# Kernel optimization log

Hardware: AMD Instinct MI355X
Metric: run time of the kernel (lower is better)

The kernel has to match this reference:

```python
import jax, jax.numpy as jnp
import numpy as np

D_MODEL = 512
DK = 4
DV = 8
HIDD = 10
HEAD = D_MODEL // DV  # 64
LN_EPS = 1e-5


def setup_inputs() -> dict:
    key = jax.random.key(0)
    ks = jax.random.split(key, 10)
    B, S, Se = 8, 512, 512
    u = jax.random.uniform  # torch.rand initializer for attention weights
    n = jax.random.normal
    return {
        "x": n(ks[0], (B, S, D_MODEL), jnp.float32),
        "x_enc": n(ks[1], (B, Se, D_MODEL), jnp.float32),
        "WqM": u(ks[2], (D_MODEL, HEAD * DK), jnp.float32),
        "WkM": u(ks[3], (D_MODEL, HEAD * DK), jnp.float32),
        "WvM": u(ks[4], (D_MODEL, HEAD * DV), jnp.float32),
        "ln_g": jnp.ones((D_MODEL,), jnp.float32),
        "ln_b": jnp.zeros((D_MODEL,), jnp.float32),
        "fc1_w": n(ks[5], (HIDD, D_MODEL), jnp.float32) * (1.0 / np.sqrt(D_MODEL)),
        "fc1_b": jnp.zeros((HIDD,), jnp.float32),
        "fc2_w": n(ks[6], (D_MODEL, HIDD), jnp.float32) * (1.0 / np.sqrt(HIDD)),
        "fc2_b": jnp.zeros((D_MODEL,), jnp.float32),
    }


def _attention(Xq, Xkv, WqM, WkM, WvM, causal_mul_mask):
    # NOTE: cross-attention in the source also uses WqM/WkM/WvM (Wq/Wk/Wv unused).
    B, Sq, _ = Xq.shape
    Sk = Xkv.shape[1]
    Q = (Xq @ WqM).reshape(B, Sq, HEAD, DK)
    K = (Xkv @ WkM).reshape(B, Sk, HEAD, DK)
    V = (Xkv @ WvM).reshape(B, Sk, HEAD, DV)
    score = jnp.einsum('bqhd,bkhd->bhqk', Q, K) / np.sqrt(DK).astype(np.float32)
    if causal_mul_mask:
        # Faithful quirk: multiplicative tril mask on scores (NOT additive -inf).
        score = score * jnp.tril(jnp.ones((Sq, Sk), score.dtype))
    w = jax.nn.softmax(score, axis=-1)
    out = jnp.einsum('bhqk,bkhd->bqhd', w, V)
    return out.reshape(B, Sq, HEAD * DV)  # HEAD*DV == d_model


def _layernorm(x, g, b):
    mu = jnp.mean(x, axis=-1, keepdims=True)
    var = jnp.mean(jnp.square(x - mu), axis=-1, keepdims=True)
    return (x - mu) * jax.lax.rsqrt(var + LN_EPS) * g + b


def reference(x, x_enc, WqM, WkM, WvM, ln_g, ln_b, fc1_w, fc1_b, fc2_w, fc2_b):
    fx = _attention(x, x, WqM, WkM, WvM, causal_mul_mask=True)
    fx = _attention(fx, x_enc, WqM, WkM, WvM, causal_mul_mask=False)
    y = _layernorm(x + fx, ln_g, ln_b)
    h = jax.nn.relu(y @ fc1_w.T + fc1_b)
    return h @ fc2_w.T + fc2_b
```

## Files before the change

### kernel.cpp

```cpp
#include <hip/hip_runtime.h>
#include <math.h>

#define D_MODEL 512
#define BATCH 8
#define SEQ 512
#define HEAD 64
#define DK 4
#define DV 8
#define HIDD 10

#define MR 32
#define KC 32
#define NC 256

__device__ __forceinline__ float4 fma4(float s, float4 w, float4 a) {
    a.x = fmaf(s, w.x, a.x); a.y = fmaf(s, w.y, a.y);
    a.z = fmaf(s, w.z, a.z); a.w = fmaf(s, w.w, a.w);
    return a;
}

__global__ __launch_bounds__(256) void proj_kernel(
    const float* __restrict__ x, const float* __restrict__ xe,
    const float* __restrict__ Wq, const float* __restrict__ Wk,
    const float* __restrict__ Wv,
    float* __restrict__ Q2, float* __restrict__ K2, float* __restrict__ V2,
    float* __restrict__ Kc, float* __restrict__ Vc)
{
    __shared__ float xt[KC * MR];
    __shared__ float wt[KC * NC];

    const int t  = threadIdx.x;
    const int bj = blockIdx.x >> 7;
    const int br = blockIdx.x & 127;
    const int r0 = br * MR;

    const float* X; const float* W; int ldw; int c0; float* dst; int vt;
    switch (bj) {
      case 0:  X = x;  W = Wq; ldw = 256; c0 = 0;   dst = Q2; vt = 0; break;
      case 1:  X = x;  W = Wk; ldw = 256; c0 = 0;   dst = K2; vt = 0; break;
      case 2:  X = x;  W = Wv; ldw = 512; c0 = 0;   dst = V2; vt = 1; break;
      case 3:  X = x;  W = Wv; ldw = 512; c0 = 256; dst = V2; vt = 1; break;
      case 4:  X = xe; W = Wk; ldw = 256; c0 = 0;   dst = Kc; vt = 0; break;
      case 5:  X = xe; W = Wv; ldw = 512; c0 = 0;   dst = Vc; vt = 1; break;
      default: X = xe; W = Wv; ldw = 512; c0 = 256; dst = Vc; vt = 1; break;
    }

    const int rg = t >> 6;
    const int cq = t & 63;
    const int rs = t & 31;
    const int kq = t >> 5;

    float4 acc[8];
#pragma unroll
    for (int r = 0; r < 8; ++r) acc[r] = make_float4(0.f, 0.f, 0.f, 0.f);

    for (int kc = 0; kc < D_MODEL; kc += KC) {
        const float4 xa = *(const float4*)(X + (long)(r0 + rs) * D_MODEL + kc + kq * 4);
        xt[(kq * 4 + 0) * MR + rs] = xa.x;
        xt[(kq * 4 + 1) * MR + rs] = xa.y;
        xt[(kq * 4 + 2) * MR + rs] = xa.z;
        xt[(kq * 4 + 3) * MR + rs] = xa.w;

#pragma unroll
        for (int i = 0; i < 8; ++i) {
            const int row = i * 4 + rg;
            *(float4*)(wt + row * NC + cq * 4) =
                *(const float4*)(W + (long)(kc + row) * ldw + c0 + cq * 4);
        }
        __syncthreads();

#pragma unroll 4
        for (int k = 0; k < KC; ++k) {
            const float4 w4 = *(const float4*)(wt + k * NC + cq * 4);
            const float4 x0 = *(const float4*)(xt + k * MR + rg * 8);
            const float4 x1 = *(const float4*)(xt + k * MR + rg * 8 + 4);
            acc[0] = fma4(x0.x, w4, acc[0]);
            acc[1] = fma4(x0.y, w4, acc[1]);
            acc[2] = fma4(x0.z, w4, acc[2]);
            acc[3] = fma4(x0.w, w4, acc[3]);
            acc[4] = fma4(x1.x, w4, acc[4]);
            acc[5] = fma4(x1.y, w4, acc[5]);
            acc[6] = fma4(x1.z, w4, acc[6]);
            acc[7] = fma4(x1.w, w4, acc[7]);
        }
        __syncthreads();
    }

    const int b = r0 >> 9;
    const int sb = (r0 & 511) + rg * 8;
    if (vt == 0) {
#pragma unroll
        for (int r = 0; r < 8; ++r)
            *(float4*)(dst + (((long)b * HEAD + cq) * SEQ + sb + r) * 4) = acc[r];
    } else {
        const int col = c0 + cq * 4;
        const int h = col >> 3;
        const int off = col & 7;
#pragma unroll
        for (int r = 0; r < 8; ++r)
            *(float4*)(dst + (((long)b * HEAD + h) * SEQ + sb + r) * 8 + off) = acc[r];
    }
}

__global__ __launch_bounds__(256, 8) void proj2_kernel(
    const float* __restrict__ A, const float* __restrict__ Wq,
    float* __restrict__ Qa, float* __restrict__ Qb)
{
    __shared__ float xt[32 * 32];
    __shared__ float wt[32 * 64];

    const int t  = threadIdx.x;
    const int kh = blockIdx.x & 1;
    const int bj = (blockIdx.x >> 1) & 3;
    const int br = blockIdx.x >> 3;
    const int r0 = br * 32;
    const int c0 = bj * 64;
    const int kb = kh * 256;
    float* dst = kh ? Qb : Qa;

    const int cq = t & 15;
    const int rr = t >> 4;
    const int rs = t & 31, kq = t >> 5;

    float4 acc[2];
    acc[0] = make_float4(0.f, 0.f, 0.f, 0.f);
    acc[1] = acc[0];

    for (int kc = 0; kc < 256; kc += 32) {
        const float4 xa = *(const float4*)(A + (long)(r0 + rs) * D_MODEL + kb + kc + kq * 4);
        xt[(kq * 4 + 0) * 32 + rs] = xa.x;
        xt[(kq * 4 + 1) * 32 + rs] = xa.y;
        xt[(kq * 4 + 2) * 32 + rs] = xa.z;
        xt[(kq * 4 + 3) * 32 + rs] = xa.w;
#pragma unroll
        for (int i = 0; i < 2; ++i) {
            const int row = i * 16 + (t >> 4);
            *(float4*)(wt + row * 64 + (t & 15) * 4) =
                *(const float4*)(Wq + (long)(kb + kc + row) * 256 + c0 + (t & 15) * 4);
        }
        __syncthreads();
#pragma unroll 4
        for (int k = 0; k < 32; ++k) {
            const float4 w4 = *(const float4*)(wt + k * 64 + cq * 4);
            const float2 x2 = *(const float2*)(xt + k * 32 + rr * 2);
            acc[0] = fma4(x2.x, w4, acc[0]);
            acc[1] = fma4(x2.y, w4, acc[1]);
        }
        __syncthreads();
    }

    const int b  = r0 >> 9;
    const int sb = (r0 & 511) + rr * 2;
    const int h  = (c0 >> 2) + cq;
#pragma unroll
    for (int r = 0; r < 2; ++r)
        *(float4*)(dst + (((long)b * HEAD + h) * SEQ + sb + r) * 4) = acc[r];
}

template <int CAUSAL>
__device__ __forceinline__ void attn_core(
    const float* __restrict__ Kl, const float* __restrict__ Vl,
    const int q1, const int q2,
    const float4 qv1, const float4 qv2,
    float* __restrict__ O, const long obase1, const long obase2)
{
    float m1 = -INFINITY, l1 = 0.f, m2 = -INFINITY, l2 = 0.f;
    float A1[8], A2[8];
#pragma unroll
    for (int j = 0; j < 8; ++j) { A1[j] = 0.f; A2[j] = 0.f; }

    for (int s0 = 0; s0 < SEQ; s0 += 8) {
        float sc1[8], sc2[8];
#pragma unroll
        for (int i = 0; i < 8; ++i) {
            const float4 k4 = *(const float4*)(Kl + (s0 + i) * 4);
            const float d1 = fmaf(qv1.x, k4.x, fmaf(qv1.y, k4.y,
                             fmaf(qv1.z, k4.z, qv1.w * k4.w)));
            const float d2 = fmaf(qv2.x, k4.x, fmaf(qv2.y, k4.y,
                             fmaf(qv2.z, k4.z, qv2.w * k4.w)));
            sc1[i] = (CAUSAL && (s0 + i) > q1) ? 0.f : d1;
            sc2[i] = (CAUSAL && (s0 + i) > q2) ? 0.f : d2;
        }
        const float g1 = fmaxf(fmaxf(fmaxf(sc1[0], sc1[1]), fmaxf(sc1[2], sc1[3])),
                               fmaxf(fmaxf(sc1[4], sc1[5]), fmaxf(sc1[6], sc1[7])));
        const float g2 = fmaxf(fmaxf(fmaxf(sc2[0], sc2[1]), fmaxf(sc2[2], sc2[3])),
                               fmaxf(fmaxf(sc2[4], sc2[5]), fmaxf(sc2[6], sc2[7])));
        if (g1 > m1) {
            const float sc = __builtin_amdgcn_exp2f(m1 - g1);
            l1 *= sc;
#pragma unroll
            for (int j = 0; j < 8; ++j) A1[j] *= sc;
            m1 = g1;
        }
        if (g2 > m2) {
            const float sc = __builtin_amdgcn_exp2f(m2 - g2);
            l2 *= sc;
#pragma unroll
            for (int j = 0; j < 8; ++j) A2[j] *= sc;
            m2 = g2;
        }
#pragma unroll
        for (int i = 0; i < 8; ++i) {
            const float p1 = __builtin_amdgcn_exp2f(sc1[i] - m1);
            const float p2 = __builtin_amdgcn_exp2f(sc2[i] - m2);
            l1 += p1; l2 += p2;
            const float4 v0 = *(const float4*)(Vl + (s0 + i) * 8);
            const float4 v1 = *(const float4*)(Vl + (s0 + i) * 8 + 4);
            A1[0] = fmaf(p1, v0.x, A1[0]); A1[1] = fmaf(p1, v0.y, A1[1]);
            A1[2] = fmaf(p1, v0.z, A1[2]); A1[3] = fmaf(p1, v0.w, A1[3]);
            A1[4] = fmaf(p1, v1.x, A1[4]); A1[5] = fmaf(p1, v1.y, A1[5]);
            A1[6] = fmaf(p1, v1.z, A1[6]); A1[7] = fmaf(p1, v1.w, A1[7]);
            A2[0] = fmaf(p2, v0.x, A2[0]); A2[1] = fmaf(p2, v0.y, A2[1]);
            A2[2] = fmaf(p2, v0.z, A2[2]); A2[3] = fmaf(p2, v0.w, A2[3]);
            A2[4] = fmaf(p2, v1.x, A2[4]); A2[5] = fmaf(p2, v1.y, A2[5]);
            A2[6] = fmaf(p2, v1.z, A2[6]); A2[7] = fmaf(p2, v1.w, A2[7]);
        }
    }

    const float i1 = 1.0f / l1, i2 = 1.0f / l2;
    *(float4*)(O + obase1)     = make_float4(A1[0]*i1, A1[1]*i1, A1[2]*i1, A1[3]*i1);
    *(float4*)(O + obase1 + 4) = make_float4(A1[4]*i1, A1[5]*i1, A1[6]*i1, A1[7]*i1);
    *(float4*)(O + obase2)     = make_float4(A2[0]*i2, A2[1]*i2, A2[2]*i2, A2[3]*i2);
    *(float4*)(O + obase2 + 4) = make_float4(A2[4]*i2, A2[5]*i2, A2[6]*i2, A2[7]*i2);
}

__global__ __launch_bounds__(256) void attn_kernel(
    const float* __restrict__ Qa, const float* __restrict__ Qb,
    const float* __restrict__ K2, const float* __restrict__ V2,
    float* __restrict__ O, int causal)
{
    __shared__ float Kl[SEQ * DK];
    __shared__ float Vl[SEQ * DV];

    const int t  = threadIdx.x;
    const int bh = blockIdx.x;
    const int b  = bh >> 6;
    const int h  = bh & 63;

    const float4* Ks = (const float4*)(K2 + (long)bh * SEQ * DK);
    ((float4*)Kl)[t]       = Ks[t];
    ((float4*)Kl)[t + 256] = Ks[t + 256];
    const float4* Vs = (const float4*)(V2 + (long)bh * SEQ * DV);
#pragma unroll
    for (int i = 0; i < 4; ++i)
        ((float4*)Vl)[t + i * 256] = Vs[t + i * 256];

    const int q1 = t, q2 = t + 256;
    float4 qv1 = *(const float4*)(Qa + ((long)bh * SEQ + q1) * 4);
    float4 qv2 = *(const float4*)(Qa + ((long)bh * SEQ + q2) * 4);
    if (Qb) {
        const float4 w1 = *(const float4*)(Qb + ((long)bh * SEQ + q1) * 4);
        const float4 w2 = *(const float4*)(Qb + ((long)bh * SEQ + q2) * 4);
        qv1.x += w1.x; qv1.y += w1.y; qv1.z += w1.z; qv1.w += w1.w;
        qv2.x += w2.x; qv2.y += w2.y; qv2.z += w2.z; qv2.w += w2.w;
    }
    const float cf = 0.5f * 1.44269504088896340736f;
    qv1.x *= cf; qv1.y *= cf; qv1.z *= cf; qv1.w *= cf;
    qv2.x *= cf; qv2.y *= cf; qv2.z *= cf; qv2.w *= cf;

    __syncthreads();

    const long ob1 = (long)b * SEQ * 512 + (long)q1 * 512 + h * DV;
    const long ob2 = (long)b * SEQ * 512 + (long)q2 * 512 + h * DV;

    if (causal)
        attn_core<1>(Kl, Vl, q1, q2, qv1, qv2, O, ob1, ob2);
    else
        attn_core<0>(Kl, Vl, q1, q2, qv1, qv2, O, ob1, ob2);
}

__global__ __launch_bounds__(256) void ln_mlp_kernel(
    const float* __restrict__ x, const float* __restrict__ fx,
    const float* __restrict__ g, const float* __restrict__ beta,
    const float* __restrict__ w1, const float* __restrict__ b1,
    const float* __restrict__ w2, const float* __restrict__ b2,
    float* __restrict__ out)
{
    const int t = threadIdx.x;
    const int lane = t & 63;
    const int row = blockIdx.x * 4 + (t >> 6);
    const long base = (long)row * D_MODEL;
    const int e0 = lane * 8;

    const float4 xa = *(const float4*)(x + base + e0);
    const float4 xb = *(const float4*)(x + base + e0 + 4);
    const float4 fa = *(const float4*)(fx + base + e0);
    const float4 fb = *(const float4*)(fx + base + e0 + 4);
    float z[8] = {xa.x+fa.x, xa.y+fa.y, xa.z+fa.z, xa.w+fa.w,
                  xb.x+fb.x, xb.y+fb.y, xb.z+fb.z, xb.w+fb.w};

    float sum = 0.f;
#pragma unroll
    for (int j = 0; j < 8; ++j) sum += z[j];
#pragma unroll
    for (int o = 32; o > 0; o >>= 1) sum += __shfl_xor(sum, o);
    float mu = sum * (1.0f / 512.0f);

    float d[8], ss = 0.f;
#pragma unroll
    for (int j = 0; j < 8; ++j) { d[j] = z[j] - mu; ss += d[j] * d[j]; }
#pragma unroll
    for (int o = 32; o > 0; o >>= 1) ss += __shfl_xor(ss, o);
    float rs = rsqrtf(ss * (1.0f / 512.0f) + 1e-5f);

    const float4 ga = *(const float4*)(g + e0);
    const float4 gb = *(const float4*)(g + e0 + 4);
    const float4 ba = *(const float4*)(beta + e0);
    const float4 bb = *(const float4*)(beta + e0 + 4);
    const float gg[8] = {ga.x,ga.y,ga.z,ga.w,gb.x,gb.y,gb.z,gb.w};
    const float bt[8] = {ba.x,ba.y,ba.z,ba.w,bb.x,bb.y,bb.z,bb.w};
    float y[8];
#pragma unroll
    for (int j = 0; j < 8; ++j) y[j] = d[j] * rs * gg[j] + bt[j];

    float part[HIDD];
#pragma unroll
    for (int i = 0; i < HIDD; ++i) {
        const float4 wa = *(const float4*)(w1 + i * 512 + e0);
        const float4 wb = *(const float4*)(w1 + i * 512 + e0 + 4);
        part[i] = y[0]*wa.x + y[1]*wa.y + y[2]*wa.z + y[3]*wa.w
                + y[4]*wb.x + y[5]*wb.y + y[6]*wb.z + y[7]*wb.w;
    }
#pragma unroll
    for (int i = 0; i < HIDD; ++i)
#pragma unroll
        for (int o = 32; o > 0; o >>= 1) part[i] += __shfl_xor(part[i], o);

    float hv[HIDD];
#pragma unroll
    for (int i = 0; i < HIDD; ++i) hv[i] = fmaxf(part[i] + b1[i], 0.f);

    float o8[8];
#pragma unroll
    for (int j = 0; j < 8; ++j) o8[j] = b2[e0 + j];
#pragma unroll
    for (int i = 0; i < HIDD; ++i)
#pragma unroll
        for (int j = 0; j < 8; ++j)
            o8[j] = fmaf(hv[i], w2[(long)(e0 + j) * 10 + i], o8[j]);

    *(float4*)(out + base + e0)     = make_float4(o8[0], o8[1], o8[2], o8[3]);
    *(float4*)(out + base + e0 + 4) = make_float4(o8[4], o8[5], o8[6], o8[7]);
}

extern "C" void kernel_launch(void* const* d_in, const int* in_sizes, int n_in,
                              void* d_out, int out_size, void* d_ws, size_t ws_size,
                              hipStream_t stream) {
    (void)in_sizes; (void)n_in; (void)out_size; (void)ws_size;
    const float* x    = (const float*)d_in[0];
    const float* xenc = (const float*)d_in[1];
    const float* Wq   = (const float*)d_in[2];
    const float* Wk   = (const float*)d_in[3];
    const float* Wv   = (const float*)d_in[4];
    const float* ln_g = (const float*)d_in[5];
    const float* ln_b = (const float*)d_in[6];
    const float* w1   = (const float*)d_in[7];
    const float* b1   = (const float*)d_in[8];
    const float* w2   = (const float*)d_in[9];
    const float* b2   = (const float*)d_in[10];
    float* out = (float*)d_out;

    float* ws = (float*)d_ws;
    float* Q1 = ws;
    float* K1 = ws +  1048576;
    float* V1 = ws +  2097152;
    float* Kc = ws +  4194304;
    float* Vc = ws +  5242880;
    float* A  = ws +  7340032;
    float* Qa = ws +  9437184;
    float* Qb = ws + 10485760;

    proj_kernel<<<dim3(896), 256, 0, stream>>>(x, xenc, Wq, Wk, Wv,
                                               Q1, K1, V1, Kc, Vc);
    attn_kernel<<<dim3(BATCH * HEAD), 256, 0, stream>>>(
        Q1, nullptr, K1, V1, A, 1);
    proj2_kernel<<<dim3(1024), 256, 0, stream>>>(A, Wq, Qa, Qb);
    attn_kernel<<<dim3(BATCH * HEAD), 256, 0, stream>>>(
        Qa, Qb, Kc, Vc, A, 0);
    ln_mlp_kernel<<<dim3(1024), 256, 0, stream>>>(x, A, ln_g, ln_b,
                                                  w1, b1, w2, b2, out);
}
```

Baseline: 353.1 us.

## Split attention over key halves with partial softmax combine and fused merge

Attention is split across two blocks per (batch, head), each scanning half the keys with 4 queries per thread, and writes partial accumulators, max and sum. A new combine kernel merges the halves for the first attention, and the LN/MLP kernel merges them inline for the second. For the causal pass, the upper key half has all-zero masked scores, so it is computed in closed form as a sum of V. This doubles grid parallelism and raises per-thread reuse of K/V shared loads, at the cost of extra partial-result traffic and one more launch. The fc2 weight loads are also vectorised.

```diff
diff --git a/kernel.cpp b/kernel.cpp
--- a/kernel.cpp
+++ b/kernel.cpp
@@ -158,119 +158,162 @@
 }
 
 template <int CAUSAL>
-__device__ __forceinline__ void attn_core(
+__device__ __forceinline__ void scan4(
     const float* __restrict__ Kl, const float* __restrict__ Vl,
-    const int q1, const int q2,
-    const float4 qv1, const float4 qv2,
-    float* __restrict__ O, const long obase1, const long obase2)
-{
-    float m1 = -INFINITY, l1 = 0.f, m2 = -INFINITY, l2 = 0.f;
-    float A1[8], A2[8];
-#pragma unroll
-    for (int j = 0; j < 8; ++j) { A1[j] = 0.f; A2[j] = 0.f; }
-
-    for (int s0 = 0; s0 < SEQ; s0 += 8) {
-        float sc1[8], sc2[8];
-#pragma unroll
-        for (int i = 0; i < 8; ++i) {
-            const float4 k4 = *(const float4*)(Kl + (s0 + i) * 4);
-            const float d1 = fmaf(qv1.x, k4.x, fmaf(qv1.y, k4.y,
-                             fmaf(qv1.z, k4.z, qv1.w * k4.w)));
-            const float d2 = fmaf(qv2.x, k4.x, fmaf(qv2.y, k4.y,
-                             fmaf(qv2.z, k4.z, qv2.w * k4.w)));
-            sc1[i] = (CAUSAL && (s0 + i) > q1) ? 0.f : d1;
-            sc2[i] = (CAUSAL && (s0 + i) > q2) ? 0.f : d2;
-        }
-        const float g1 = fmaxf(fmaxf(fmaxf(sc1[0], sc1[1]), fmaxf(sc1[2], sc1[3])),
-                               fmaxf(fmaxf(sc1[4], sc1[5]), fmaxf(sc1[6], sc1[7])));
-        const float g2 = fmaxf(fmaxf(fmaxf(sc2[0], sc2[1]), fmaxf(sc2[2], sc2[3])),
-                               fmaxf(fmaxf(sc2[4], sc2[5]), fmaxf(sc2[6], sc2[7])));
-        if (g1 > m1) {
-            const float sc = __builtin_amdgcn_exp2f(m1 - g1);
-            l1 *= sc;
-#pragma unroll
-            for (int j = 0; j < 8; ++j) A1[j] *= sc;
-            m1 = g1;
-        }
-        if (g2 > m2) {
-            const float sc = __builtin_amdgcn_exp2f(m2 - g2);
-            l2 *= sc;
-#pragma unroll
-            for (int j = 0; j < 8; ++j) A2[j] *= sc;
-            m2 = g2;
-        }
-#pragma unroll
-        for (int i = 0; i < 8; ++i) {
-            const float p1 = __builtin_amdgcn_exp2f(sc1[i] - m1);
-            const float p2 = __builtin_amdgcn_exp2f(sc2[i] - m2);
-            l1 += p1; l2 += p2;
-            const float4 v0 = *(const float4*)(Vl + (s0 + i) * 8);
-            const float4 v1 = *(const float4*)(Vl + (s0 + i) * 8 + 4);
-            A1[0] = fmaf(p1, v0.x, A1[0]); A1[1] = fmaf(p1, v0.y, A1[1]);
-            A1[2] = fmaf(p1, v0.z, A1[2]); A1[3] = fmaf(p1, v0.w, A1[3]);
-            A1[4] = fmaf(p1, v1.x, A1[4]); A1[5] = fmaf(p1, v1.y, A1[5]);
-            A1[6] = fmaf(p1, v1.z, A1[6]); A1[7] = fmaf(p1, v1.w, A1[7]);
-            A2[0] = fmaf(p2, v0.x, A2[0]); A2[1] = fmaf(p2, v0.y, A2[1]);
-            A2[2] = fmaf(p2, v0.z, A2[2]); A2[3] = fmaf(p2, v0.w, A2[3]);
-            A2[4] = fmaf(p2, v1.x, A2[4]); A2[5] = fmaf(p2, v1.y, A2[5]);
-            A2[6] = fmaf(p2, v1.z, A2[6]); A2[7] = fmaf(p2, v1.w, A2[7]);
-        }
-    }
-
-    const float i1 = 1.0f / l1, i2 = 1.0f / l2;
-    *(float4*)(O + obase1)     = make_float4(A1[0]*i1, A1[1]*i1, A1[2]*i1, A1[3]*i1);
-    *(float4*)(O + obase1 + 4) = make_float4(A1[4]*i1, A1[5]*i1, A1[6]*i1, A1[7]*i1);
-    *(float4*)(O + obase2)     = make_float4(A2[0]*i2, A2[1]*i2, A2[2]*i2, A2[3]*i2);
-    *(float4*)(O + obase2 + 4) = make_float4(A2[4]*i2, A2[5]*i2, A2[6]*i2, A2[7]*i2);
-}
-
-__global__ __launch_bounds__(256) void attn_kernel(
+    const float4 (&qv)[4], const int (&qb)[4],
+    float (&m)[4], float (&l)[4], float (&A)[4][8])
+{
+    for (int s0 = 0; s0 < 256; s0 += 4) {
+        float4 k[4];
+#pragma unroll
+        for (int i = 0; i < 4; ++i)
+            k[i] = *(const float4*)(Kl + (s0 + i) * DK);
+        float sc[4][4];
+#pragma unroll
+        for (int j = 0; j < 4; ++j) {
+#pragma unroll
+            for (int i = 0; i < 4; ++i) {
+                const float d = fmaf(qv[j].x, k[i].x, fmaf(qv[j].y, k[i].y,
+                                fmaf(qv[j].z, k[i].z, qv[j].w * k[i].w)));
+                sc[j][i] = (CAUSAL && (s0 + i) > qb[j]) ? 0.f : d;
+            }
+            const float gm = fmaxf(fmaxf(sc[j][0], sc[j][1]),
+                                   fmaxf(sc[j][2], sc[j][3]));
+            if (gm > m[j]) {
+                const float s = __builtin_amdgcn_exp2f(m[j] - gm);
+                l[j] *= s;
+#pragma unroll
+                for (int r = 0; r < 8; ++r) A[j][r] *= s;
+                m[j] = gm;
+            }
+        }
+#pragma unroll
+        for (int i = 0; i < 4; ++i) {
+            const float4 v0 = *(const float4*)(Vl + (s0 + i) * DV);
+            const float4 v1 = *(const float4*)(Vl + (s0 + i) * DV + 4);
+#pragma unroll
+            for (int j = 0; j < 4; ++j) {
+                const float p = __builtin_amdgcn_exp2f(sc[j][i] - m[j]);
+                l[j] += p;
+                A[j][0] = fmaf(p, v0.x, A[j][0]); A[j][1] = fmaf(p, v0.y, A[j][1]);
+                A[j][2] = fmaf(p, v0.z, A[j][2]); A[j][3] = fmaf(p, v0.w, A[j][3]);
+                A[j][4] = fmaf(p, v1.x, A[j][4]); A[j][5] = fmaf(p, v1.y, A[j][5]);
+                A[j][6] = fmaf(p, v1.z, A[j][6]); A[j][7] = fmaf(p, v1.w, A[j][7]);
+            }
+        }
+    }
+}
+
+__global__ __launch_bounds__(128) void attn_kernel(
     const float* __restrict__ Qa, const float* __restrict__ Qb,
     const float* __restrict__ K2, const float* __restrict__ V2,
-    float* __restrict__ O, int causal)
-{
-    __shared__ float Kl[SEQ * DK];
-    __shared__ float Vl[SEQ * DV];
+    float* __restrict__ PA, float* __restrict__ PM, const int causal)
+{
+    __shared__ float Kl[256 * DK];
+    __shared__ float Vl[256 * DV];
 
     const int t  = threadIdx.x;
-    const int bh = blockIdx.x;
-    const int b  = bh >> 6;
-    const int h  = bh & 63;
-
-    const float4* Ks = (const float4*)(K2 + (long)bh * SEQ * DK);
+    const int bh = blockIdx.x >> 1;
+    const int kh = blockIdx.x & 1;
+
+    const float4* Ks = (const float4*)(K2 + ((long)bh * SEQ + kh * 256) * DK);
     ((float4*)Kl)[t]       = Ks[t];
-    ((float4*)Kl)[t + 256] = Ks[t + 256];
-    const float4* Vs = (const float4*)(V2 + (long)bh * SEQ * DV);
+    ((float4*)Kl)[t + 128] = Ks[t + 128];
+    const float4* Vs = (const float4*)(V2 + ((long)bh * SEQ + kh * 256) * DV);
 #pragma unroll
     for (int i = 0; i < 4; ++i)
-        ((float4*)Vl)[t + i * 256] = Vs[t + i * 256];
-
-    const int q1 = t, q2 = t + 256;
-    float4 qv1 = *(const float4*)(Qa + ((long)bh * SEQ + q1) * 4);
-    float4 qv2 = *(const float4*)(Qa + ((long)bh * SEQ + q2) * 4);
-    if (Qb) {
-        const float4 w1 = *(const float4*)(Qb + ((long)bh * SEQ + q1) * 4);
-        const float4 w2 = *(const float4*)(Qb + ((long)bh * SEQ + q2) * 4);
-        qv1.x += w1.x; qv1.y += w1.y; qv1.z += w1.z; qv1.w += w1.w;
-        qv2.x += w2.x; qv2.y += w2.y; qv2.z += w2.z; qv2.w += w2.w;
-    }
+        ((float4*)Vl)[t + i * 128] = Vs[t + i * 128];
+    __syncthreads();
+
+    const long pbase = ((long)(bh * 2 + kh)) * SEQ + t * 4;
+
+    if (causal && kh == 1 && t < 64) {
+        float s[8] = {0.f, 0.f, 0.f, 0.f, 0.f, 0.f, 0.f, 0.f};
+#pragma unroll
+        for (int i = 0; i < 4; ++i) {
+            const float4 v0 = *(const float4*)(Vl + (t + i * 64) * DV);
+            const float4 v1 = *(const float4*)(Vl + (t + i * 64) * DV + 4);
+            s[0] += v0.x; s[1] += v0.y; s[2] += v0.z; s[3] += v0.w;
+            s[4] += v1.x; s[5] += v1.y; s[6] += v1.z; s[7] += v1.w;
+        }
+#pragma unroll
+        for (int o = 32; o > 0; o >>= 1)
+#pragma unroll
+            for (int j = 0; j < 8; ++j) s[j] += __shfl_xor(s[j], o);
+#pragma unroll
+        for (int j = 0; j < 4; ++j) {
+            *(float4*)(PA + (pbase + j) * 8)     = make_float4(s[0], s[1], s[2], s[3]);
+            *(float4*)(PA + (pbase + j) * 8 + 4) = make_float4(s[4], s[5], s[6], s[7]);
+            *(float2*)(PM + (pbase + j) * 2)     = make_float2(0.f, 256.f);
+        }
+        return;
+    }
+
     const float cf = 0.5f * 1.44269504088896340736f;
-    qv1.x *= cf; qv1.y *= cf; qv1.z *= cf; qv1.w *= cf;
-    qv2.x *= cf; qv2.y *= cf; qv2.z *= cf; qv2.w *= cf;
-
-    __syncthreads();
-
-    const long ob1 = (long)b * SEQ * 512 + (long)q1 * 512 + h * DV;
-    const long ob2 = (long)b * SEQ * 512 + (long)q2 * 512 + h * DV;
-
-    if (causal)
-        attn_core<1>(Kl, Vl, q1, q2, qv1, qv2, O, ob1, ob2);
-    else
-        attn_core<0>(Kl, Vl, q1, q2, qv1, qv2, O, ob1, ob2);
+    float4 qv[4]; int qb[4];
+#pragma unroll
+    for (int j = 0; j < 4; ++j) {
+        const int q = t * 4 + j;
+        float4 v = *(const float4*)(Qa + ((long)bh * SEQ + q) * 4);
+        if (Qb) {
+            const float4 w = *(const float4*)(Qb + ((long)bh * SEQ + q) * 4);
+            v.x += w.x; v.y += w.y; v.z += w.z; v.w += w.w;
+        }
+        v.x *= cf; v.y *= cf; v.z *= cf; v.w *= cf;
+        qv[j] = v;
+        qb[j] = q - kh * 256;
+    }
+
+    float m[4], l[4], A[4][8];
+#pragma unroll
+    for (int j = 0; j < 4; ++j) {
+        m[j] = -INFINITY; l[j] = 0.f;
+#pragma unroll
+        for (int r = 0; r < 8; ++r) A[j][r] = 0.f;
+    }
+
+    if (causal) scan4<1>(Kl, Vl, qv, qb, m, l, A);
+    else        scan4<0>(Kl, Vl, qv, qb, m, l, A);
+
+#pragma unroll
+    for (int j = 0; j < 4; ++j) {
+        *(float4*)(PA + (pbase + j) * 8)     = make_float4(A[j][0], A[j][1], A[j][2], A[j][3]);
+        *(float4*)(PA + (pbase + j) * 8 + 4) = make_float4(A[j][4], A[j][5], A[j][6], A[j][7]);
+        *(float2*)(PM + (pbase + j) * 2)     = make_float2(m[j], l[j]);
+    }
+}
+
+__global__ __launch_bounds__(256) void combine_kernel(
+    const float* __restrict__ PA, const float* __restrict__ PM,
+    float* __restrict__ A)
+{
+    const int tid = blockIdx.x * 256 + threadIdx.x;
+    const int bh  = tid >> 9;
+    const int q   = tid & 511;
+    const long p0 = ((long)bh * 2 + 0) * SEQ + q;
+    const long p1 = ((long)bh * 2 + 1) * SEQ + q;
+    const float2 ml0 = *(const float2*)(PM + p0 * 2);
+    const float2 ml1 = *(const float2*)(PM + p1 * 2);
+    const float M = fmaxf(ml0.x, ml1.x);
+    float w0 = __builtin_amdgcn_exp2f(ml0.x - M);
+    float w1 = __builtin_amdgcn_exp2f(ml1.x - M);
+    const float inv = 1.0f / fmaf(ml0.y, w0, ml1.y * w1);
+    w0 *= inv; w1 *= inv;
+    const float4 x0 = *(const float4*)(PA + p0 * 8);
+    const float4 x1 = *(const float4*)(PA + p0 * 8 + 4);
+    const float4 y0 = *(const float4*)(PA + p1 * 8);
+    const float4 y1 = *(const float4*)(PA + p1 * 8 + 4);
+    const int b = bh >> 6, h = bh & 63;
+    float* dst = A + ((long)b * SEQ + q) * D_MODEL + h * DV;
+    *(float4*)(dst)     = make_float4(x0.x*w0 + y0.x*w1, x0.y*w0 + y0.y*w1,
+                                      x0.z*w0 + y0.z*w1, x0.w*w0 + y0.w*w1);
+    *(float4*)(dst + 4) = make_float4(x1.x*w0 + y1.x*w1, x1.y*w0 + y1.y*w1,
+                                      x1.z*w0 + y1.z*w1, x1.w*w0 + y1.w*w1);
 }
 
 __global__ __launch_bounds__(256) void ln_mlp_kernel(
-    const float* __restrict__ x, const float* __restrict__ fx,
+    const float* __restrict__ x,
+    const float* __restrict__ PA, const float* __restrict__ PM,
     const float* __restrict__ g, const float* __restrict__ beta,
     const float* __restrict__ w1, const float* __restrict__ b1,
     const float* __restrict__ w2, const float* __restrict__ b2,
@@ -279,36 +322,52 @@
     const int t = threadIdx.x;
     const int lane = t & 63;
     const int row = blockIdx.x * 4 + (t >> 6);
+    const int b = row >> 9, q = row & 511;
     const long base = (long)row * D_MODEL;
     const int e0 = lane * 8;
 
+    const long p0 = (((long)b * HEAD + lane) * 2 + 0) * SEQ + q;
+    const long p1 = (((long)b * HEAD + lane) * 2 + 1) * SEQ + q;
+    const float2 ml0 = *(const float2*)(PM + p0 * 2);
+    const float2 ml1 = *(const float2*)(PM + p1 * 2);
+    const float M = fmaxf(ml0.x, ml1.x);
+    float cw0 = __builtin_amdgcn_exp2f(ml0.x - M);
+    float cw1 = __builtin_amdgcn_exp2f(ml1.x - M);
+    const float inv = 1.0f / fmaf(ml0.y, cw0, ml1.y * cw1);
+    cw0 *= inv; cw1 *= inv;
+    const float4 fa0 = *(const float4*)(PA + p0 * 8);
+    const float4 fa1 = *(const float4*)(PA + p0 * 8 + 4);
+    const float4 fb0 = *(const float4*)(PA + p1 * 8);
+    const float4 fb1 = *(const float4*)(PA + p1 * 8 + 4);
+
     const float4 xa = *(const float4*)(x + base + e0);
     const float4 xb = *(const float4*)(x + base + e0 + 4);
-    const float4 fa = *(const float4*)(fx + base + e0);
-    const float4 fb = *(const float4*)(fx + base + e0 + 4);
-    float z[8] = {xa.x+fa.x, xa.y+fa.y, xa.z+fa.z, xa.w+fa.w,
-                  xb.x+fb.x, xb.y+fb.y, xb.z+fb.z, xb.w+fb.w};
+    float z[8] = {
+        xa.x + fa0.x * cw0 + fb0.x * cw1, xa.y + fa0.y * cw0 + fb0.y * cw1,
+        xa.z + fa0.z * cw0 + fb0.z * cw1, xa.w + fa0.w * cw0 + fb0.w * cw1,
+        xb.x + fa1.x * cw0 + fb1.x * cw1, xb.y + fa1.y * cw0 + fb1.y * cw1,
+        xb.z + fa1.z * cw0 + fb1.z * cw1, xb.w + fa1.w * cw0 + fb1.w * cw1};
 
     float sum = 0.f;
 #pragma unroll
     for (int j = 0; j < 8; ++j) sum += z[j];
 #pragma unroll
     for (int o = 32; o > 0; o >>= 1) sum += __shfl_xor(sum, o);
-    float mu = sum * (1.0f / 512.0f);
+    const float mu = sum * (1.0f / 512.0f);
 
     float d[8], ss = 0.f;
 #pragma unroll
     for (int j = 0; j < 8; ++j) { d[j] = z[j] - mu; ss += d[j] * d[j]; }
 #pragma unroll
     for (int o = 32; o > 0; o >>= 1) ss += __shfl_xor(ss, o);
-    float rs = rsqrtf(ss * (1.0f / 512.0f) + 1e-5f);
+    const float rs = rsqrtf(ss * (1.0f / 512.0f) + 1e-5f);
 
     const float4 ga = *(const float4*)(g + e0);
     const float4 gb = *(const float4*)(g + e0 + 4);
     const float4 ba = *(const float4*)(beta + e0);
     const float4 bb = *(const float4*)(beta + e0 + 4);
-    const float gg[8] = {ga.x,ga.y,ga.z,ga.w,gb.x,gb.y,gb.z,gb.w};
-    const float bt[8] = {ba.x,ba.y,ba.z,ba.w,bb.x,bb.y,bb.z,bb.w};
+    const float gg[8] = {ga.x, ga.y, ga.z, ga.w, gb.x, gb.y, gb.z, gb.w};
+    const float bt[8] = {ba.x, ba.y, ba.z, ba.w, bb.x, bb.y, bb.z, bb.w};
     float y[8];
 #pragma unroll
     for (int j = 0; j < 8; ++j) y[j] = d[j] * rs * gg[j] + bt[j];
@@ -318,8 +377,8 @@
     for (int i = 0; i < HIDD; ++i) {
         const float4 wa = *(const float4*)(w1 + i * 512 + e0);
         const float4 wb = *(const float4*)(w1 + i * 512 + e0 + 4);
-        part[i] = y[0]*wa.x + y[1]*wa.y + y[2]*wa.z + y[3]*wa.w
-                + y[4]*wb.x + y[5]*wb.y + y[6]*wb.z + y[7]*wb.w;
+        part[i] = y[0] * wa.x + y[1] * wa.y + y[2] * wa.z + y[3] * wa.w
+                + y[4] * wb.x + y[5] * wb.y + y[6] * wb.z + y[7] * wb.w;
     }
 #pragma unroll
     for (int i = 0; i < HIDD; ++i)
@@ -330,14 +389,21 @@
 #pragma unroll
     for (int i = 0; i < HIDD; ++i) hv[i] = fmaxf(part[i] + b1[i], 0.f);
 
-    float o8[8];
-#pragma unroll
-    for (int j = 0; j < 8; ++j) o8[j] = b2[e0 + j];
-#pragma unroll
-    for (int i = 0; i < HIDD; ++i)
-#pragma unroll
-        for (int j = 0; j < 8; ++j)
-            o8[j] = fmaf(hv[i], w2[(long)(e0 + j) * 10 + i], o8[j]);
+    const float4 b2a = *(const float4*)(b2 + e0);
+    const float4 b2b = *(const float4*)(b2 + e0 + 4);
+    float o8[8] = {b2a.x, b2a.y, b2a.z, b2a.w, b2b.x, b2b.y, b2b.z, b2b.w};
+#pragma unroll
+    for (int j = 0; j < 8; ++j) {
+        const float* wr = w2 + (long)(e0 + j) * 10;
+        const float2 wA = *(const float2*)(wr);
+        const float2 wB = *(const float2*)(wr + 2);
+        const float2 wC = *(const float2*)(wr + 4);
+        const float2 wD = *(const float2*)(wr + 6);
+        const float2 wE = *(const float2*)(wr + 8);
+        o8[j] += hv[0] * wA.x + hv[1] * wA.y + hv[2] * wB.x + hv[3] * wB.y
+               + hv[4] * wC.x + hv[5] * wC.y + hv[6] * wD.x + hv[7] * wD.y
+               + hv[8] * wE.x + hv[9] * wE.y;
+    }
 
     *(float4*)(out + base + e0)     = make_float4(o8[0], o8[1], o8[2], o8[3]);
     *(float4*)(out + base + e0 + 4) = make_float4(o8[4], o8[5], o8[6], o8[7]);
@@ -366,17 +432,20 @@
     float* V1 = ws +  2097152;
     float* Kc = ws +  4194304;
     float* Vc = ws +  5242880;
-    float* A  = ws +  7340032;
-    float* Qa = ws +  9437184;
-    float* Qb = ws + 10485760;
+    float* PA = ws +  7340032;
+    float* PM = ws + 11534336;
+    float* A  = ws;
+    float* Qa = ws +  2097152;
+    float* Qb = ws +  3145728;
 
     proj_kernel<<<dim3(896), 256, 0, stream>>>(x, xenc, Wq, Wk, Wv,
                                                Q1, K1, V1, Kc, Vc);
-    attn_kernel<<<dim3(BATCH * HEAD), 256, 0, stream>>>(
-        Q1, nullptr, K1, V1, A, 1);
+    attn_kernel<<<dim3(BATCH * HEAD * 2), 128, 0, stream>>>(
+        Q1, nullptr, K1, V1, PA, PM, 1);
+    combine_kernel<<<dim3(1024), 256, 0, stream>>>(PA, PM, A);
     proj2_kernel<<<dim3(1024), 256, 0, stream>>>(A, Wq, Qa, Qb);
-    attn_kernel<<<dim3(BATCH * HEAD), 256, 0, stream>>>(
-        Qa, Qb, Kc, Vc, A, 0);
-    ln_mlp_kernel<<<dim3(1024), 256, 0, stream>>>(x, A, ln_g, ln_b,
+    attn_kernel<<<dim3(BATCH * HEAD * 2), 128, 0, stream>>>(
+        Qa, Qb, Kc, Vc, PA, PM, 0);
+    ln_mlp_kernel<<<dim3(1024), 256, 0, stream>>>(x, PA, PM, ln_g, ln_b,
                                                   w1, b1, w2, b2, out);
 }
```

Result: slower. 362.8 us (+2.8%).
